# Kernel optimization log

Hardware: AMD Instinct MI355X
Metric: run time of the kernel (lower is better)

The kernel has to match this reference:

```python
import jax, jax.numpy as jnp
import numpy as np


def _hardswish(x):
    return x * jnp.clip(x + 3.0, 0.0, 6.0) / 6.0


def _rel_coords_table(W):
    # [1, 2W-1, 2W-1, 2], log-spaced continuous relative coords (SwinV2)
    rc = jnp.arange(-(W - 1), W, dtype=jnp.float32)
    grid = jnp.stack(jnp.meshgrid(rc, rc, indexing='ij'), axis=-1)[None]
    grid = grid / float(W - 1) * 8.0
    return jnp.sign(grid) * jnp.log2(jnp.abs(grid) + 1.0) / np.float32(np.log2(8.0))


def _rel_pos_index(W):
    # [N, N] int indices into the (2W-1)^2 bias table
    coords = np.stack(np.meshgrid(np.arange(W), np.arange(W), indexing='ij')).reshape(2, -1)
    rel = (coords[:, :, None] - coords[:, None, :]).transpose(1, 2, 0)  # [N, N, 2]
    rel[:, :, 0] += W - 1
    rel[:, :, 1] += W - 1
    rel[:, :, 0] *= 2 * W - 1
    return jnp.asarray(rel.sum(-1))


def setup_inputs() -> dict:
    key = jax.random.key(0)
    ks = jax.random.split(key, 6)
    dim, num_heads, W = 512, 16, 8
    N = W * W
    B, nW = 2048, 64
    return {
        'x': jax.random.normal(ks[0], (B, N, dim), jnp.float32),
        'mask': jax.random.normal(ks[1], (nW, N, N), jnp.float32),
        'w_qkv': jax.random.normal(ks[2], (dim, 3 * dim), jnp.float32) * 0.02,
        'w_out': jax.random.normal(ks[3], (dim, dim), jnp.float32) * 0.02,
        'cpb_w1': jax.random.normal(ks[4], (2, 512), jnp.float32) * 0.02,
        'cpb_w2': jax.random.normal(ks[5], (512, num_heads), jnp.float32) * 0.02,
        'logits_scale': jnp.log(10.0 * jnp.ones((num_heads, 1, 1), jnp.float32)),
        'window_size': W,
        'num_heads': num_heads,
    }


def reference(x, mask, w_qkv, w_out, cpb_w1, cpb_w2, logits_scale, window_size, num_heads):
    B, N, C = x.shape
    hd = C // num_heads
    qkv = (x @ w_qkv).reshape(B, N, 3, num_heads, hd).transpose(2, 0, 3, 1, 4)
    q, k, v = qkv[0], qkv[1], qkv[2]  # [B, H, N, hd]

    # cosine attention (L2-normalized q, k) with clamped learned logit scale
    qn = q / jnp.clip(jnp.linalg.norm(q, axis=-1, keepdims=True), 1e-12)
    kn = k / jnp.clip(jnp.linalg.norm(k, axis=-1, keepdims=True), 1e-12)
    attn = jnp.einsum('bhnd,bhmd->bhnm', qn, kn)
    scale = jnp.exp(jnp.minimum(logits_scale, jnp.log(jnp.float32(100.0))))  # [H,1,1]
    attn = attn * scale[None]

    # continuous position bias via tiny MLP + index gather, sigmoid-scaled
    table = _rel_coords_table(window_size)                       # [1, 2W-1, 2W-1, 2]
    bias_table = (_hardswish(table @ cpb_w1) @ cpb_w2).reshape(-1, num_heads)
    idx = _rel_pos_index(window_size)                            # [N, N]
    bias = bias_table[idx.reshape(-1)].reshape(N, N, num_heads).transpose(2, 0, 1)
    attn = attn + 16.0 * jax.nn.sigmoid(bias)[None]

    if mask is not None:
        nW = mask.shape[0]
        attn = attn.reshape(B // nW, nW, num_heads, N, N) + mask[None, :, None]
        attn = attn.reshape(B, num_heads, N, N)

    # NOTE: original uses nn.Softmax(1) -> softmax over the HEAD axis; replicate faithfully
    attn = jax.nn.softmax(attn, axis=1)

    out = jnp.einsum('bhnm,bhmd->bhnd', attn, v).transpose(0, 2, 1, 3).reshape(B, N, C)
    return out @ w_out
```

## Files before the change

kernel.cpp:

```cpp
#include <hip/hip_runtime.h>
#include <hip/hip_bf16.h>

typedef unsigned short u16;
typedef unsigned int u32;
typedef __attribute__((ext_vector_type(8))) short bf16x8;
typedef __attribute__((ext_vector_type(4))) float f32x4;
typedef __attribute__((ext_vector_type(4))) float float4v;

__device__ __forceinline__ float bf2f(u16 v) {
  union { u32 u; float f; } x; x.u = ((u32)v) << 16; return x.f;
}
__device__ __forceinline__ u16 f2bf(float f) {
  union { u32 u; float f; } x; x.f = f;
  return (u16)((x.u + 0x7fffu + ((x.u >> 16) & 1u)) >> 16);
}

__device__ __forceinline__ void gload16(const void* g, void* l) {
  __builtin_amdgcn_global_load_lds(
      (const __attribute__((address_space(1))) u32*)g,
      (__attribute__((address_space(3))) u32*)l, 16, 0, 0);
}

#define MFMA16(a, bfr, cacc) __builtin_amdgcn_mfma_f32_16x16x32_bf16((a), (bfr), (cacc), 0, 0, 0)


__global__ void convert_bf16_kernel(const float* __restrict__ in,
                                    u16* __restrict__ out, int n8) {
  int t = blockIdx.x * blockDim.x + threadIdx.x;
  if (t >= n8) return;
  const float4v* p = (const float4v*)(in + (size_t)t * 8);
  float4v a = p[0], b = p[1];
  union { bf16x8 v; u16 s[8]; } o;
  o.s[0] = f2bf(a[0]); o.s[1] = f2bf(a[1]); o.s[2] = f2bf(a[2]); o.s[3] = f2bf(a[3]);
  o.s[4] = f2bf(b[0]); o.s[5] = f2bf(b[1]); o.s[6] = f2bf(b[2]); o.s[7] = f2bf(b[3]);
  *(bf16x8*)(out + (size_t)t * 8) = o.v;
}

__global__ void transpose_kernel(const float* __restrict__ in, u16* __restrict__ out,
                                 int R, int C) {
  int t = blockIdx.x * blockDim.x + threadIdx.x;
  if (t >= R * C) return;
  int c = t / R, r = t % R;
  out[t] = f2bf(in[r * C + c]);
}

__global__ void bias_tab_kernel(const float* __restrict__ w1, const float* __restrict__ w2,
                                float* __restrict__ tab) {
  int t = blockIdx.x * blockDim.x + threadIdx.x;
  if (t >= 225 * 16) return;
  int r = t >> 4, h = t & 15;
  int i = r / 15, j = r % 15;
  float gi = (float)(i - 7) * (8.0f / 7.0f);
  float gj = (float)(j - 7) * (8.0f / 7.0f);
  float si = (gi > 0.f) ? 1.f : ((gi < 0.f) ? -1.f : 0.f);
  float sj = (gj > 0.f) ? 1.f : ((gj < 0.f) ? -1.f : 0.f);
  float t0 = si * log2f(fabsf(gi) + 1.0f) * (1.0f / 3.0f);
  float t1 = sj * log2f(fabsf(gj) + 1.0f) * (1.0f / 3.0f);
  float acc = 0.f;
  for (int k = 0; k < 512; ++k) {
    float a = t0 * w1[k] + t1 * w1[512 + k];
    float hs = a * fminf(fmaxf(a + 3.f, 0.f), 6.f) * (1.f / 6.f);
    acc += hs * w2[k * 16 + h];
  }
  tab[t] = acc;
}

__global__ void bias16_kernel(const float* __restrict__ tab, float* __restrict__ b16) {
  int t = blockIdx.x * blockDim.x + threadIdx.x;
  if (t >= 16 * 64 * 64) return;
  int h = t >> 12, nm = t & 4095, n = nm >> 6, m = nm & 63;
  int idx = ((n >> 3) - (m >> 3) + 7) * 15 + ((n & 7) - (m & 7) + 7);
  float b = tab[idx * 16 + h];
  b16[t] = 16.0f / (1.0f + expf(-b));
}

template <bool F32OUT>
__global__ __launch_bounds__(256) void gemm_bt(const u16* __restrict__ A,
                                               const u16* __restrict__ Bt,
                                               void* __restrict__ Cout,
                                               int M, int N, int K) {
  __shared__ u16 lA[128 * 64];
  __shared__ u16 lB[128 * 64];
  const int tid = threadIdx.x;
  const int w = tid >> 6, l = tid & 63;
  const int lg = l >> 4, li = l & 15;
  const int nbn = N >> 7;
  const int nwg = gridDim.x;
  int bidx = blockIdx.x;
  int q = nwg >> 3, r = nwg & 7;
  int xcd = bidx & 7, pos = bidx >> 3;
  int swz = (xcd < r ? xcd * (q + 1) : r * (q + 1) + (xcd - r) * q) + pos;
  int bm = swz / nbn, bn = swz % nbn;
  const int wr = w >> 1, wc = w & 1;

  f32x4 acc[4][4];
#pragma unroll
  for (int i = 0; i < 4; i++)
#pragma unroll
    for (int j = 0; j < 4; j++) acc[i][j] = (f32x4){0.f, 0.f, 0.f, 0.f};

  const u16* Abase = A + (size_t)(bm * 128) * K;
  const u16* Bbase = Bt + (size_t)(bn * 128) * K;

  for (int k0 = 0; k0 < K; k0 += 64) {
#pragma unroll
    for (int i = 0; i < 4; ++i) {
      int c = w * 256 + i * 64 + l;
      int row = c >> 3, kc = c & 7;
      int kcs = kc ^ (row & 7);
      gload16(Abase + (size_t)row * K + k0 + kcs * 8, (u16*)lA + c * 8);
      gload16(Bbase + (size_t)row * K + k0 + kcs * 8, (u16*)lB + c * 8);
    }
    __syncthreads();
#pragma unroll
    for (int kk = 0; kk < 2; ++kk) {
      bf16x8 af[4], bfr[4];
#pragma unroll
      for (int t = 0; t < 4; ++t) {
        int row = wr * 64 + t * 16 + li;
        af[t] = *(const bf16x8*)&lA[row * 64 + (((kk * 4 + lg) ^ (row & 7)) << 3)];
        int col = wc * 64 + t * 16 + li;
        bfr[t] = *(const bf16x8*)&lB[col * 64 + (((kk * 4 + lg) ^ (col & 7)) << 3)];
      }
#pragma unroll
      for (int tm = 0; tm < 4; ++tm)
#pragma unroll
        for (int tn = 0; tn < 4; ++tn)
          acc[tm][tn] = MFMA16(af[tm], bfr[tn], acc[tm][tn]);
    }
    __syncthreads();
  }
  int r0 = bm * 128 + wr * 64 + lg * 4;
  int c0 = bn * 128 + wc * 64 + li;
#pragma unroll
  for (int tm = 0; tm < 4; ++tm)
#pragma unroll
    for (int tn = 0; tn < 4; ++tn)
#pragma unroll
      for (int j = 0; j < 4; ++j) {
        size_t off = (size_t)(r0 + tm * 16 + j) * N + c0 + tn * 16;
        if (F32OUT)
          ((float*)Cout)[off] = acc[tm][tn][j];
        else
          ((u16*)Cout)[off] = f2bf(acc[tm][tn][j]);
      }
}

__global__ __launch_bounds__(256) void gemm_qkv(const u16* __restrict__ A,
                                                const u16* __restrict__ Bt,
                                                u16* __restrict__ Cq,
                                                const float* __restrict__ lscale,
                                                int M, int K) {
  __shared__ u16 lds[128 * 136];
  u16* lA = lds;
  u16* lB = lds + 8192;
  const int tid = threadIdx.x;
  const int w = tid >> 6, l = tid & 63;
  const int lg = l >> 4, li = l & 15;
  const int nbn = 12;
  const int nwg = gridDim.x;
  int bidx = blockIdx.x;
  int q = nwg >> 3, r = nwg & 7;
  int xcd = bidx & 7, pos = bidx >> 3;
  int swz = (xcd < r ? xcd * (q + 1) : r * (q + 1) + (xcd - r) * q) + pos;
  int bm = swz / nbn, bn = swz % nbn;
  const int wr = w >> 1, wc = w & 1;

  f32x4 acc[4][4];
#pragma unroll
  for (int i = 0; i < 4; i++)
#pragma unroll
    for (int j = 0; j < 4; j++) acc[i][j] = (f32x4){0.f, 0.f, 0.f, 0.f};

  const u16* Abase = A + (size_t)(bm * 128) * K;
  const u16* Bbase = Bt + (size_t)(bn * 128) * K;

  for (int k0 = 0; k0 < K; k0 += 64) {
#pragma unroll
    for (int i = 0; i < 4; ++i) {
      int c = w * 256 + i * 64 + l;
      int row = c >> 3, kc = c & 7;
      int kcs = kc ^ (row & 7);
      gload16(Abase + (size_t)row * K + k0 + kcs * 8, lA + c * 8);
      gload16(Bbase + (size_t)row * K + k0 + kcs * 8, lB + c * 8);
    }
    __syncthreads();
#pragma unroll
    for (int kk = 0; kk < 2; ++kk) {
      bf16x8 af[4], bfr[4];
#pragma unroll
      for (int t = 0; t < 4; ++t) {
        int row = wr * 64 + t * 16 + li;
        af[t] = *(const bf16x8*)&lA[row * 64 + (((kk * 4 + lg) ^ (row & 7)) << 3)];
        int col = wc * 64 + t * 16 + li;
        bfr[t] = *(const bf16x8*)&lB[col * 64 + (((kk * 4 + lg) ^ (col & 7)) << 3)];
      }
#pragma unroll
      for (int tm = 0; tm < 4; ++tm)
#pragma unroll
        for (int tn = 0; tn < 4; ++tn)
          acc[tm][tn] = MFMA16(af[tm], bfr[tn], acc[tm][tn]);
    }
    __syncthreads();
  }

  const int s_t = bn >> 2;
  const int hq = (bn & 3) * 4;
  float scv[2];
  if (s_t == 0) {
    scv[0] = __expf(fminf(lscale[hq + wc * 2 + 0], 4.6051702f));
    scv[1] = __expf(fminf(lscale[hq + wc * 2 + 1], 4.6051702f));
  } else {
    scv[0] = scv[1] = 1.0f;
  }
  if (s_t < 2) {
#pragma unroll
    for (int tm = 0; tm < 4; ++tm)
#pragma unroll
      for (int g = 0; g < 2; ++g) {
        f32x4 s2;
#pragma unroll
        for (int j = 0; j < 4; ++j)
          s2[j] = acc[tm][2 * g][j] * acc[tm][2 * g][j] +
                  acc[tm][2 * g + 1][j] * acc[tm][2 * g + 1][j];
#pragma unroll
        for (int m = 1; m <= 8; m <<= 1)
#pragma unroll
          for (int j = 0; j < 4; ++j) s2[j] += __shfl_xor(s2[j], m);
#pragma unroll
        for (int j = 0; j < 4; ++j) {
          float rn = scv[g] / fmaxf(sqrtf(s2[j]), 1e-12f);
          acc[tm][2 * g][j] *= rn;
          acc[tm][2 * g + 1][j] *= rn;
        }
      }
  }
  u16* ct = lds;
#pragma unroll
  for (int tm = 0; tm < 4; ++tm)
#pragma unroll
    for (int tn = 0; tn < 4; ++tn)
#pragma unroll
      for (int j = 0; j < 4; ++j)
        ct[(wr * 64 + tm * 16 + lg * 4 + j) * 136 + wc * 64 + tn * 16 + li] =
            f2bf(acc[tm][tn][j]);
  __syncthreads();
  {
    int rr = tid >> 2;
    int c8 = (tid & 3) * 8;
#pragma unroll
    for (int bh = 0; bh < 2; ++bh)
#pragma unroll
      for (int ht = 0; ht < 4; ++ht) {
        bf16x8 v = *(const bf16x8*)(ct + (bh * 64 + rr) * 136 + ht * 32 + c8);
        size_t base = ((size_t)(s_t * 16 + hq + ht) * 2048 + (bm * 2 + bh)) * 2048;
        *(bf16x8*)(Cq + base + rr * 32 + c8) = v;
      }
  }
}

__global__ __launch_bounds__(512, 2) void attn2(const u16* __restrict__ qkv,
                                                const float* __restrict__ mask,
                                                const float* __restrict__ bias16,
                                                u16* __restrict__ aout) {
  __shared__ float S[16 * 16 * 65];
  u16* P16 = (u16*)S;
  float* ob = S;
  const int tid = threadIdx.x;
  const int w = tid >> 6, l = tid & 63;
  const int lg = l >> 4, li = l & 15;
  const int b = blockIdx.x, wm = b & 63;
  const float* mask_w = mask + wm * 4096;

  f32x4 oacc[2][4][2];
#pragma unroll
  for (int hp = 0; hp < 2; ++hp)
#pragma unroll
    for (int i = 0; i < 4; ++i) {
      oacc[hp][i][0] = (f32x4){0.f, 0.f, 0.f, 0.f};
      oacc[hp][i][1] = (f32x4){0.f, 0.f, 0.f, 0.f};
    }

#pragma unroll
  for (int c = 0; c < 4; ++c) {
#pragma unroll
    for (int hp = 0; hp < 2; ++hp) {
      int h = w + hp * 8;
      const u16* qb = qkv + ((size_t)h * 2048 + b) * 2048;
      const u16* kb = qkv + ((size_t)(16 + h) * 2048 + b) * 2048;
      const float* bias_h = bias16 + h * 4096;
      bf16x8 kfc = *(const bf16x8*)(kb + (c * 16 + li) * 32 + lg * 8);
      int mg = c * 16 + li;
#pragma unroll
      for (int tn = 0; tn < 4; ++tn) {
        bf16x8 qt = *(const bf16x8*)(qb + (tn * 16 + li) * 32 + lg * 8);
        f32x4 z = {0.f, 0.f, 0.f, 0.f};
        f32x4 s = MFMA16(qt, kfc, z);
#pragma unroll
        for (int j = 0; j < 4; ++j) {
          int n = tn * 16 + lg * 4 + j;
          S[h * 1040 + li * 65 + n] = s[j] + bias_h[n * 64 + mg] + mask_w[n * 64 + mg];
        }
      }
    }
    __syncthreads();
#pragma unroll
    for (int pp = 0; pp < 2; ++pp) {
      int p = tid + pp * 512;
      int base = (p >> 6) * 65 + (p & 63);
      float mx = -3.0e38f;
#pragma unroll
      for (int hh = 0; hh < 16; ++hh) mx = fmaxf(mx, S[hh * 1040 + base]);
      float sum = 0.f;
#pragma unroll
      for (int hh = 0; hh < 16; ++hh) {
        float e = __expf(S[hh * 1040 + base] - mx);
        S[hh * 1040 + base] = e;
        sum += e;
      }
      float inv = 1.0f / sum;
#pragma unroll
      for (int hh = 0; hh < 16; ++hh)
        P16[(hh * 1040 + base) * 2] = f2bf(S[hh * 1040 + base] * inv);
    }
    __syncthreads();
#pragma unroll
    for (int hp = 0; hp < 2; ++hp) {
      int h = w + hp * 8;
      const u16* vb = qkv + ((size_t)(32 + h) * 2048 + b) * 2048;
      bf16x8 vf[2];
#pragma unroll
      for (int td = 0; td < 2; ++td)
#pragma unroll
        for (int e = 0; e < 8; ++e)
          vf[td][e] = (lg < 2)
                          ? (short)vb[(c * 16 + lg * 8 + e) * 32 + td * 16 + li]
                          : (short)0;
#pragma unroll
      for (int tn = 0; tn < 4; ++tn) {
        bf16x8 pf;
#pragma unroll
        for (int e = 0; e < 8; ++e)
          pf[e] = (lg < 2)
                      ? (short)P16[(h * 1040 + (lg * 8 + e) * 65 + tn * 16 + li) * 2]
                      : (short)0;
        oacc[hp][tn][0] = MFMA16(pf, vf[0], oacc[hp][tn][0]);
        oacc[hp][tn][1] = MFMA16(pf, vf[1], oacc[hp][tn][1]);
      }
    }
    __syncthreads();
  }

#pragma unroll
  for (int tn = 0; tn < 4; ++tn) {
#pragma unroll
    for (int hp = 0; hp < 2; ++hp) {
      int h = w + hp * 8;
#pragma unroll
      for (int td = 0; td < 2; ++td)
#pragma unroll
        for (int j = 0; j < 4; ++j)
          ob[(lg * 4 + j) * 516 + h * 32 + td * 16 + li] = oacc[hp][tn][td][j];
    }
    __syncthreads();
    {
      int rr = tid >> 5, c16 = (tid & 31) * 16;
      const float* src = ob + rr * 516 + c16;
      u16* dst = aout + ((size_t)b * 64 + tn * 16 + rr) * 512 + c16;
#pragma unroll
      for (int half = 0; half < 2; ++half) {
        union { bf16x8 v; u16 u[8]; } o;
#pragma unroll
        for (int e = 0; e < 8; ++e) o.u[e] = f2bf(src[half * 8 + e]);
        *(bf16x8*)(dst + half * 8) = o.v;
      }
    }
    __syncthreads();
  }
}

extern "C" void kernel_launch(void* const* d_in, const int* in_sizes, int n_in,
                              void* d_out, int out_size, void* d_ws, size_t ws_size,
                              hipStream_t stream) {
  const float* x = (const float*)d_in[0];
  const float* mask = (const float*)d_in[1];
  const float* w_qkv = (const float*)d_in[2];
  const float* w_out = (const float*)d_in[3];
  const float* cpb_w1 = (const float*)d_in[4];
  const float* cpb_w2 = (const float*)d_in[5];
  const float* lscale = (const float*)d_in[6];
  float* out = (float*)d_out;

  char* ws = (char*)d_ws;
  u16* wqkvT = (u16*)ws;
  u16* woutT = (u16*)(ws + 1572864ull);
  float* btab = (float*)(ws + 2097152ull);
  float* b16 = (float*)(ws + 2113536ull);
  u16* qkv_ws = (u16*)(ws + 2375680ull);
  u16* xb = (u16*)(ws + 2375680ull + 402653184ull);
  u16* attn_out = xb;

  transpose_kernel<<<(512 * 1536 + 255) / 256, 256, 0, stream>>>(w_qkv, wqkvT, 512, 1536);
  transpose_kernel<<<(512 * 512 + 255) / 256, 256, 0, stream>>>(w_out, woutT, 512, 512);
  bias_tab_kernel<<<(225 * 16 + 255) / 256, 256, 0, stream>>>(cpb_w1, cpb_w2, btab);
  bias16_kernel<<<(16 * 64 * 64 + 255) / 256, 256, 0, stream>>>(btab, b16);

  convert_bf16_kernel<<<(131072 * 64 + 255) / 256, 256, 0, stream>>>(x, xb, 131072 * 64);

  gemm_qkv<<<12288, 256, 0, stream>>>(xb, wqkvT, qkv_ws, lscale, 131072, 512);

  attn2<<<2048, 512, 0, stream>>>(qkv_ws, mask, b16, attn_out);

  gemm_bt<true><<<4096, 256, 0, stream>>>(attn_out, woutT, out, 131072, 512, 512);
}
```

Before: 944.7 us.

## Rewrite QKV GEMM as 256x256 tile, 8-wave kernel with double-buffered LDS

Replaces the 128x128, 4-wave QKV projection GEMM with a 256x256 tile kernel that uses 8 waves, each computing 128x64. LDS is double-buffered so the next K tile's global-to-LDS loads overlap the MFMAs on the current tile, and B fragments are reused across two A sub-phases. s_setprio is raised around the MFMA bursts. The larger tile halves the global traffic per FLOP, but it uses about 136KB of LDS and 128 accumulator registers per thread, which may limit occupancy to one block per CU despite the launch bound of 2.

```diff
diff --git a/kernel.cpp b/kernel.cpp
--- a/kernel.cpp
+++ b/kernel.cpp
@@ -146,116 +146,138 @@
       }
 }
 
-__global__ __launch_bounds__(256) void gemm_qkv(const u16* __restrict__ A,
-                                                const u16* __restrict__ Bt,
-                                                u16* __restrict__ Cq,
-                                                const float* __restrict__ lscale,
-                                                int M, int K) {
-  __shared__ u16 lds[128 * 136];
-  u16* lA = lds;
-  u16* lB = lds + 8192;
+__device__ __forceinline__ void stage_round(const u16* __restrict__ srcb, int tile,
+                                            int r, int tid, u16* dst) {
+  int c = r * 512 + tid;
+  int row = c >> 3;
+  int kcs = (c & 7) ^ (row & 7);
+  gload16(srcb + (size_t)row * 512 + tile * 64 + kcs * 8, dst + c * 8);
+}
+
+template <int QM, int KS, bool READB>
+__device__ __forceinline__ void phase_op(const u16* curA, const u16* curB,
+                                         int wm, int wn, int lg, int li,
+                                         bf16x8 (&bc)[4], f32x4 (&acc)[8][4]) {
+  bf16x8 af[4];
+#pragma unroll
+  for (int i = 0; i < 4; ++i) {
+    int row = wm * 128 + (QM * 4 + i) * 16 + li;
+    af[i] = *(const bf16x8*)&curA[row * 64 + (((KS * 4 + lg) ^ (row & 7)) << 3)];
+  }
+  if (READB) {
+#pragma unroll
+    for (int nt = 0; nt < 4; ++nt) {
+      int col = wn * 64 + nt * 16 + li;
+      bc[nt] = *(const bf16x8*)&curB[col * 64 + (((KS * 4 + lg) ^ (col & 7)) << 3)];
+    }
+  }
+  __builtin_amdgcn_s_setprio(1);
+#pragma unroll
+  for (int i = 0; i < 4; ++i)
+#pragma unroll
+    for (int nt = 0; nt < 4; ++nt)
+      acc[QM * 4 + i][nt] = MFMA16(af[i], bc[nt], acc[QM * 4 + i][nt]);
+  __builtin_amdgcn_s_setprio(0);
+}
+
+__global__ __launch_bounds__(512, 2) void gemm_qkv256(
+    const u16* __restrict__ A, const u16* __restrict__ Bt,
+    u16* __restrict__ Cq, const float* __restrict__ lscale) {
+  __shared__ u16 lds[69632];
   const int tid = threadIdx.x;
-  const int w = tid >> 6, l = tid & 63;
+  const int l = tid & 63, w = tid >> 6;
   const int lg = l >> 4, li = l & 15;
-  const int nbn = 12;
-  const int nwg = gridDim.x;
+  const int wm = w >> 2, wn = w & 3;
   int bidx = blockIdx.x;
-  int q = nwg >> 3, r = nwg & 7;
-  int xcd = bidx & 7, pos = bidx >> 3;
-  int swz = (xcd < r ? xcd * (q + 1) : r * (q + 1) + (xcd - r) * q) + pos;
-  int bm = swz / nbn, bn = swz % nbn;
-  const int wr = w >> 1, wc = w & 1;
-
-  f32x4 acc[4][4];
-#pragma unroll
-  for (int i = 0; i < 4; i++)
-#pragma unroll
-    for (int j = 0; j < 4; j++) acc[i][j] = (f32x4){0.f, 0.f, 0.f, 0.f};
-
-  const u16* Abase = A + (size_t)(bm * 128) * K;
-  const u16* Bbase = Bt + (size_t)(bn * 128) * K;
-
-  for (int k0 = 0; k0 < K; k0 += 64) {
-#pragma unroll
-    for (int i = 0; i < 4; ++i) {
-      int c = w * 256 + i * 64 + l;
-      int row = c >> 3, kc = c & 7;
-      int kcs = kc ^ (row & 7);
-      gload16(Abase + (size_t)row * K + k0 + kcs * 8, lA + c * 8);
-      gload16(Bbase + (size_t)row * K + k0 + kcs * 8, lB + c * 8);
-    }
-    __syncthreads();
-#pragma unroll
-    for (int kk = 0; kk < 2; ++kk) {
-      bf16x8 af[4], bfr[4];
-#pragma unroll
-      for (int t = 0; t < 4; ++t) {
-        int row = wr * 64 + t * 16 + li;
-        af[t] = *(const bf16x8*)&lA[row * 64 + (((kk * 4 + lg) ^ (row & 7)) << 3)];
-        int col = wc * 64 + t * 16 + li;
-        bfr[t] = *(const bf16x8*)&lB[col * 64 + (((kk * 4 + lg) ^ (col & 7)) << 3)];
-      }
-#pragma unroll
-      for (int tm = 0; tm < 4; ++tm)
-#pragma unroll
-        for (int tn = 0; tn < 4; ++tn)
-          acc[tm][tn] = MFMA16(af[tm], bfr[tn], acc[tm][tn]);
-    }
-    __syncthreads();
-  }
-
-  const int s_t = bn >> 2;
-  const int hq = (bn & 3) * 4;
-  float scv[2];
-  if (s_t == 0) {
-    scv[0] = __expf(fminf(lscale[hq + wc * 2 + 0], 4.6051702f));
-    scv[1] = __expf(fminf(lscale[hq + wc * 2 + 1], 4.6051702f));
-  } else {
-    scv[0] = scv[1] = 1.0f;
-  }
+  int swz = (bidx & 7) * (gridDim.x >> 3) + (bidx >> 3);
+  int bm = swz / 6, bn = swz % 6;
+  const u16* Ab = A + (size_t)bm * 256 * 512;
+  const u16* Bb = Bt + (size_t)bn * 256 * 512;
+
+  f32x4 acc[8][4];
+#pragma unroll
+  for (int i = 0; i < 8; ++i)
+#pragma unroll
+    for (int j = 0; j < 4; ++j) acc[i][j] = (f32x4){0.f, 0.f, 0.f, 0.f};
+
+#pragma unroll
+  for (int r = 0; r < 4; ++r) stage_round(Ab, 0, r, tid, lds);
+#pragma unroll
+  for (int r = 0; r < 4; ++r) stage_round(Bb, 0, r, tid, lds + 32768);
+  asm volatile("s_waitcnt vmcnt(0)" ::: "memory");
+  __builtin_amdgcn_s_barrier();
+
+#pragma unroll 1
+  for (int t = 0; t < 8; ++t) {
+    const int s = t & 1;
+    u16* curA = lds + s * 16384;
+    u16* curB = lds + 32768 + s * 16384;
+    u16* nxtA = lds + (s ^ 1) * 16384;
+    u16* nxtB = lds + 32768 + (s ^ 1) * 16384;
+    if (t < 7) {
+#pragma unroll
+      for (int r = 0; r < 4; ++r) stage_round(Ab, t + 1, r, tid, nxtA);
+#pragma unroll
+      for (int r = 0; r < 4; ++r) stage_round(Bb, t + 1, r, tid, nxtB);
+    }
+    bf16x8 bc[4];
+    phase_op<0, 0, true >(curA, curB, wm, wn, lg, li, bc, acc);
+    phase_op<1, 0, false>(curA, curB, wm, wn, lg, li, bc, acc);
+    phase_op<0, 1, true >(curA, curB, wm, wn, lg, li, bc, acc);
+    phase_op<1, 1, false>(curA, curB, wm, wn, lg, li, bc, acc);
+    asm volatile("s_waitcnt vmcnt(0)" ::: "memory");
+    __builtin_amdgcn_s_barrier();
+  }
+  __syncthreads();
+
+  const int s_t = bn >> 1;
+  const int h0 = (bn & 1) * 8;
   if (s_t < 2) {
 #pragma unroll
-    for (int tm = 0; tm < 4; ++tm)
-#pragma unroll
-      for (int g = 0; g < 2; ++g) {
+    for (int g = 0; g < 2; ++g) {
+      float sca = 1.0f;
+      if (s_t == 0) sca = __expf(fminf(lscale[h0 + wn * 2 + g], 4.6051702f));
+#pragma unroll
+      for (int mt = 0; mt < 8; ++mt) {
         f32x4 s2;
 #pragma unroll
         for (int j = 0; j < 4; ++j)
-          s2[j] = acc[tm][2 * g][j] * acc[tm][2 * g][j] +
-                  acc[tm][2 * g + 1][j] * acc[tm][2 * g + 1][j];
+          s2[j] = acc[mt][2 * g][j] * acc[mt][2 * g][j] +
+                  acc[mt][2 * g + 1][j] * acc[mt][2 * g + 1][j];
 #pragma unroll
         for (int m = 1; m <= 8; m <<= 1)
 #pragma unroll
           for (int j = 0; j < 4; ++j) s2[j] += __shfl_xor(s2[j], m);
 #pragma unroll
         for (int j = 0; j < 4; ++j) {
-          float rn = scv[g] / fmaxf(sqrtf(s2[j]), 1e-12f);
-          acc[tm][2 * g][j] *= rn;
-          acc[tm][2 * g + 1][j] *= rn;
+          float rn = sca / fmaxf(sqrtf(s2[j]), 1e-12f);
+          acc[mt][2 * g][j] *= rn;
+          acc[mt][2 * g + 1][j] *= rn;
         }
       }
-  }
+    }
+  }
+
   u16* ct = lds;
 #pragma unroll
-  for (int tm = 0; tm < 4; ++tm)
-#pragma unroll
-    for (int tn = 0; tn < 4; ++tn)
+  for (int mt = 0; mt < 8; ++mt)
+#pragma unroll
+    for (int nt = 0; nt < 4; ++nt)
 #pragma unroll
       for (int j = 0; j < 4; ++j)
-        ct[(wr * 64 + tm * 16 + lg * 4 + j) * 136 + wc * 64 + tn * 16 + li] =
-            f2bf(acc[tm][tn][j]);
+        ct[(wm * 128 + mt * 16 + lg * 4 + j) * 272 + wn * 64 + nt * 16 + li] =
+            f2bf(acc[mt][nt][j]);
   __syncthreads();
-  {
-    int rr = tid >> 2;
-    int c8 = (tid & 3) * 8;
-#pragma unroll
-    for (int bh = 0; bh < 2; ++bh)
-#pragma unroll
-      for (int ht = 0; ht < 4; ++ht) {
-        bf16x8 v = *(const bf16x8*)(ct + (bh * 64 + rr) * 136 + ht * 32 + c8);
-        size_t base = ((size_t)(s_t * 16 + hq + ht) * 2048 + (bm * 2 + bh)) * 2048;
-        *(bf16x8*)(Cq + base + rr * 32 + c8) = v;
-      }
+#pragma unroll
+  for (int r = 0; r < 16; ++r) {
+    int id = r * 512 + tid;
+    int blk = id >> 8;
+    int wi = blk >> 3, ht = blk & 7;
+    int off = id & 255;
+    int rw = off >> 2, d8 = (off & 3) * 8;
+    bf16x8 v = *(const bf16x8*)&ct[(wi * 64 + rw) * 272 + ht * 32 + d8];
+    size_t base = ((size_t)(s_t * 16 + h0 + ht) * 2048 + (bm * 4 + wi)) * 2048;
+    *(bf16x8*)(Cq + base + rw * 32 + d8) = v;
   }
 }
 
@@ -407,7 +429,7 @@
 
   convert_bf16_kernel<<<(131072 * 64 + 255) / 256, 256, 0, stream>>>(x, xb, 131072 * 64);
 
-  gemm_qkv<<<12288, 256, 0, stream>>>(xb, wqkvT, qkv_ws, lscale, 131072, 512);
+  gemm_qkv256<<<3072, 512, 0, stream>>>(xb, wqkvT, qkv_ws, lscale);
 
   attn2<<<2048, 512, 0, stream>>>(qkv_ws, mask, b16, attn_out);
 
```

After: 949.1 us. Within noise of the previous version (+0.5%).

## Store V transposed from QKV GEMM epilogue and vectorize V loads in attention

Applied to the files above, without the earlier changes.

The QKV GEMM epilogue now writes the V section transposed (d-major, n contiguous) through a transposed LDS staging tile. This lets the attention kernel load V fragments with single 16-byte vector loads instead of eight scalar gathers. It also hoists the Q fragments out of the chunk loop, keeps softmax values in registers instead of re-reading LDS, and precomputes GEMM load addresses. The transposed LDS write pattern may cause bank conflicts, and the Q fragments held across the loop raise register pressure.

```diff
diff --git a/kernel.cpp b/kernel.cpp
--- a/kernel.cpp
+++ b/kernel.cpp
@@ -175,14 +175,26 @@
   const u16* Abase = A + (size_t)(bm * 128) * K;
   const u16* Bbase = Bt + (size_t)(bn * 128) * K;
 
+  const u16* srcA[4];
+  const u16* srcB[4];
+  u16* dstA[4];
+  u16* dstB[4];
+#pragma unroll
+  for (int i = 0; i < 4; ++i) {
+    int c = w * 256 + i * 64 + l;
+    int row = c >> 3, kc = c & 7;
+    int kcs = kc ^ (row & 7);
+    srcA[i] = Abase + (size_t)row * K + kcs * 8;
+    srcB[i] = Bbase + (size_t)row * K + kcs * 8;
+    dstA[i] = lA + c * 8;
+    dstB[i] = lB + c * 8;
+  }
+
   for (int k0 = 0; k0 < K; k0 += 64) {
 #pragma unroll
     for (int i = 0; i < 4; ++i) {
-      int c = w * 256 + i * 64 + l;
-      int row = c >> 3, kc = c & 7;
-      int kcs = kc ^ (row & 7);
-      gload16(Abase + (size_t)row * K + k0 + kcs * 8, lA + c * 8);
-      gload16(Bbase + (size_t)row * K + k0 + kcs * 8, lB + c * 8);
+      gload16(srcA[i] + k0, dstA[i]);
+      gload16(srcB[i] + k0, dstB[i]);
     }
     __syncthreads();
 #pragma unroll
@@ -206,14 +218,14 @@
 
   const int s_t = bn >> 2;
   const int hq = (bn & 3) * 4;
-  float scv[2];
-  if (s_t == 0) {
-    scv[0] = __expf(fminf(lscale[hq + wc * 2 + 0], 4.6051702f));
-    scv[1] = __expf(fminf(lscale[hq + wc * 2 + 1], 4.6051702f));
-  } else {
-    scv[0] = scv[1] = 1.0f;
-  }
   if (s_t < 2) {
+    float scv[2];
+    if (s_t == 0) {
+      scv[0] = __expf(fminf(lscale[hq + wc * 2 + 0], 4.6051702f));
+      scv[1] = __expf(fminf(lscale[hq + wc * 2 + 1], 4.6051702f));
+    } else {
+      scv[0] = scv[1] = 1.0f;
+    }
 #pragma unroll
     for (int tm = 0; tm < 4; ++tm)
 #pragma unroll
@@ -234,28 +246,50 @@
           acc[tm][2 * g + 1][j] *= rn;
         }
       }
-  }
-  u16* ct = lds;
-#pragma unroll
-  for (int tm = 0; tm < 4; ++tm)
-#pragma unroll
-    for (int tn = 0; tn < 4; ++tn)
-#pragma unroll
-      for (int j = 0; j < 4; ++j)
-        ct[(wr * 64 + tm * 16 + lg * 4 + j) * 136 + wc * 64 + tn * 16 + li] =
-            f2bf(acc[tm][tn][j]);
-  __syncthreads();
-  {
-    int rr = tid >> 2;
-    int c8 = (tid & 3) * 8;
-#pragma unroll
-    for (int bh = 0; bh < 2; ++bh)
-#pragma unroll
-      for (int ht = 0; ht < 4; ++ht) {
-        bf16x8 v = *(const bf16x8*)(ct + (bh * 64 + rr) * 136 + ht * 32 + c8);
-        size_t base = ((size_t)(s_t * 16 + hq + ht) * 2048 + (bm * 2 + bh)) * 2048;
-        *(bf16x8*)(Cq + base + rr * 32 + c8) = v;
-      }
+    u16* ct = lds;
+#pragma unroll
+    for (int tm = 0; tm < 4; ++tm)
+#pragma unroll
+      for (int tn = 0; tn < 4; ++tn)
+#pragma unroll
+        for (int j = 0; j < 4; ++j)
+          ct[(wr * 64 + tm * 16 + lg * 4 + j) * 136 + wc * 64 + tn * 16 + li] =
+              f2bf(acc[tm][tn][j]);
+    __syncthreads();
+    {
+      int rr = tid >> 2;
+      int c8 = (tid & 3) * 8;
+#pragma unroll
+      for (int bh = 0; bh < 2; ++bh)
+#pragma unroll
+        for (int ht = 0; ht < 4; ++ht) {
+          bf16x8 v = *(const bf16x8*)(ct + (bh * 64 + rr) * 136 + ht * 32 + c8);
+          size_t base = ((size_t)(s_t * 16 + hq + ht) * 2048 + (bm * 2 + bh)) * 2048;
+          *(bf16x8*)(Cq + base + rr * 32 + c8) = v;
+        }
+    }
+  } else {
+    u16* ctT = lds;
+#pragma unroll
+    for (int tm = 0; tm < 4; ++tm)
+#pragma unroll
+      for (int tn = 0; tn < 4; ++tn)
+#pragma unroll
+        for (int j = 0; j < 4; ++j)
+          ctT[(wc * 64 + tn * 16 + li) * 136 + wr * 64 + tm * 16 + lg * 4 + j] =
+              f2bf(acc[tm][tn][j]);
+    __syncthreads();
+#pragma unroll
+    for (int r2 = 0; r2 < 8; ++r2) {
+      int id = r2 * 256 + tid;
+      int colc = id >> 4;
+      int seg = id & 15;
+      bf16x8 v = *(const bf16x8*)&ctT[colc * 136 + seg * 8];
+      int ht = colc >> 5, d = colc & 31;
+      int wi = seg >> 3, n0 = (seg & 7) * 8;
+      size_t base = ((size_t)(32 + hq + ht) * 2048 + (bm * 2 + wi)) * 2048;
+      *(bf16x8*)(Cq + base + d * 64 + n0) = v;
+    }
   }
 }
 
@@ -272,6 +306,15 @@
   const int b = blockIdx.x, wm = b & 63;
   const float* mask_w = mask + wm * 4096;
 
+  bf16x8 qfr[2][4];
+#pragma unroll
+  for (int hp = 0; hp < 2; ++hp) {
+    const u16* qb = qkv + ((size_t)(w + hp * 8) * 2048 + b) * 2048;
+#pragma unroll
+    for (int tn = 0; tn < 4; ++tn)
+      qfr[hp][tn] = *(const bf16x8*)(qb + (tn * 16 + li) * 32 + lg * 8);
+  }
+
   f32x4 oacc[2][4][2];
 #pragma unroll
   for (int hp = 0; hp < 2; ++hp)
@@ -286,16 +329,14 @@
 #pragma unroll
     for (int hp = 0; hp < 2; ++hp) {
       int h = w + hp * 8;
-      const u16* qb = qkv + ((size_t)h * 2048 + b) * 2048;
       const u16* kb = qkv + ((size_t)(16 + h) * 2048 + b) * 2048;
       const float* bias_h = bias16 + h * 4096;
       bf16x8 kfc = *(const bf16x8*)(kb + (c * 16 + li) * 32 + lg * 8);
       int mg = c * 16 + li;
 #pragma unroll
       for (int tn = 0; tn < 4; ++tn) {
-        bf16x8 qt = *(const bf16x8*)(qb + (tn * 16 + li) * 32 + lg * 8);
         f32x4 z = {0.f, 0.f, 0.f, 0.f};
-        f32x4 s = MFMA16(qt, kfc, z);
+        f32x4 s = MFMA16(qfr[hp][tn], kfc, z);
 #pragma unroll
         for (int j = 0; j < 4; ++j) {
           int n = tn * 16 + lg * 4 + j;
@@ -308,34 +349,41 @@
     for (int pp = 0; pp < 2; ++pp) {
       int p = tid + pp * 512;
       int base = (p >> 6) * 65 + (p & 63);
+      float vals[16];
       float mx = -3.0e38f;
 #pragma unroll
-      for (int hh = 0; hh < 16; ++hh) mx = fmaxf(mx, S[hh * 1040 + base]);
+      for (int hh = 0; hh < 16; ++hh) {
+        vals[hh] = S[hh * 1040 + base];
+        mx = fmaxf(mx, vals[hh]);
+      }
       float sum = 0.f;
 #pragma unroll
       for (int hh = 0; hh < 16; ++hh) {
-        float e = __expf(S[hh * 1040 + base] - mx);
-        S[hh * 1040 + base] = e;
+        float e = __expf(vals[hh] - mx);
+        vals[hh] = e;
         sum += e;
       }
       float inv = 1.0f / sum;
 #pragma unroll
       for (int hh = 0; hh < 16; ++hh)
-        P16[(hh * 1040 + base) * 2] = f2bf(S[hh * 1040 + base] * inv);
+        P16[(hh * 1040 + base) * 2] = f2bf(vals[hh] * inv);
     }
     __syncthreads();
 #pragma unroll
     for (int hp = 0; hp < 2; ++hp) {
       int h = w + hp * 8;
-      const u16* vb = qkv + ((size_t)(32 + h) * 2048 + b) * 2048;
+      const u16* vbT = qkv + ((size_t)(32 + h) * 2048 + b) * 2048;
       bf16x8 vf[2];
-#pragma unroll
-      for (int td = 0; td < 2; ++td)
-#pragma unroll
-        for (int e = 0; e < 8; ++e)
-          vf[td][e] = (lg < 2)
-                          ? (short)vb[(c * 16 + lg * 8 + e) * 32 + td * 16 + li]
-                          : (short)0;
+      if (lg < 2) {
+#pragma unroll
+        for (int td = 0; td < 2; ++td)
+          vf[td] = *(const bf16x8*)(vbT + (td * 16 + li) * 64 + c * 16 + lg * 8);
+      } else {
+#pragma unroll
+        for (int td = 0; td < 2; ++td)
+#pragma unroll
+          for (int e = 0; e < 8; ++e) vf[td][e] = 0;
+      }
 #pragma unroll
       for (int tn = 0; tn < 4; ++tn) {
         bf16x8 pf;
```

Result: no change. 959.4 us (+1.6%).
